# Kernel optimization log

Measured on AMD Instinct MI355X. Metric: run time of the kernel, lower is better.

The kernel has to match this reference:

```python
import jax, jax.numpy as jnp
import numpy as np

EMBED_DIM = 1024
HEADS = 16
HEAD_DIM = EMBED_DIM // HEADS


def setup_inputs() -> dict:
    key = jax.random.key(0)
    ks = jax.random.split(key, 9)
    D = EMBED_DIM
    s = 1.0 / np.sqrt(D)
    x = jax.random.normal(ks[0], (4, 2048, D), dtype=jnp.float32)
    Wq = jax.random.uniform(ks[1], (D, D), jnp.float32, -s, s)
    bq = jnp.zeros((D,), jnp.float32)
    Wk = jax.random.uniform(ks[2], (D, D), jnp.float32, -s, s)
    bk = jnp.zeros((D,), jnp.float32)
    Wv = jax.random.uniform(ks[3], (D, D), jnp.float32, -s, s)
    bv = jnp.zeros((D,), jnp.float32)
    Wo = jax.random.uniform(ks[4], (D, D), jnp.float32, -s, s)
    bo = jnp.zeros((D,), jnp.float32)
    gamma = jnp.ones((D,), jnp.float32)
    beta = jnp.zeros((D,), jnp.float32)
    return {"x": x, "Wq": Wq, "bq": bq, "Wk": Wk, "bk": bk,
            "Wv": Wv, "bv": bv, "Wo": Wo, "bo": bo,
            "gamma": gamma, "beta": beta}


def reference(x, Wq, bq, Wk, bk, Wv, bv, Wo, bo, gamma, beta):
    B, S, D = x.shape
    H, Dh = HEADS, HEAD_DIM
    # projections -> [B, H, S, Dh]
    q = (x @ Wq + bq).reshape(B, S, H, Dh).transpose(0, 2, 1, 3)
    k = (x @ Wk + bk).reshape(B, S, H, Dh).transpose(0, 2, 1, 3)
    v = (x @ Wv + bv).reshape(B, S, H, Dh).transpose(0, 2, 1, 3)
    scores = jnp.einsum('bhqd,bhkd->bhqk', q, k) / jnp.sqrt(jnp.float32(Dh))
    attn = jax.nn.softmax(scores, axis=-1)  # dropout is identity in eval
    ctx = jnp.einsum('bhqk,bhkd->bhqd', attn, v)
    ctx = ctx.transpose(0, 2, 1, 3).reshape(B, S, D)
    out = ctx @ Wo + bo
    # residual + LayerNorm (eps=1e-5, torch default)
    h = out + x
    mu = jnp.mean(h, axis=-1, keepdims=True)
    var = jnp.mean(jnp.square(h - mu), axis=-1, keepdims=True)
    return (h - mu) * jax.lax.rsqrt(var + 1e-5) * gamma + beta
```

## Files before the change

### kernel.cpp

```cpp
#include <hip/hip_runtime.h>
#include <hip/hip_bf16.h>
#include <stdint.h>

typedef short sh4 __attribute__((ext_vector_type(4)));
typedef short sh8 __attribute__((ext_vector_type(8)));
typedef float fl4 __attribute__((ext_vector_type(4)));
typedef float f32x4 __attribute__((ext_vector_type(4)));
typedef float f32x16 __attribute__((ext_vector_type(16)));
typedef uint32_t u32x4 __attribute__((ext_vector_type(4)));

static __device__ __forceinline__ short f2bf(float f) {
  union { float f; uint32_t u; } v;
  v.f = f;
  uint32_t r = v.u + 0x7fffu + ((v.u >> 16) & 1u);
  return (short)(r >> 16);
}

static __device__ __forceinline__ uint32_t cvt_pk_bf16(float a, float b) {
  uint32_t r;
  asm("v_cvt_pk_bf16_f32 %0, %1, %2" : "=v"(r) : "v"(a), "v"(b));
  return r;
}

static __device__ __forceinline__ void pl32swap(uint32_t& a, uint32_t& b) {
  asm volatile("v_permlane32_swap_b32 %0, %1" : "+v"(a), "+v"(b));
}

static __device__ __forceinline__ void gload_lds16(const void* g, void* l) {
  __builtin_amdgcn_global_load_lds((const __attribute__((address_space(1))) void*)g,
                                   (__attribute__((address_space(3))) void*)l, 16, 0, 0);
}

__global__ __launch_bounds__(256) void k_wt(const float* __restrict__ Wq, const float* __restrict__ Wk,
                                            const float* __restrict__ Wv, const float* __restrict__ Wo,
                                            short* __restrict__ Tq, short* __restrict__ Tk,
                                            short* __restrict__ Tv, short* __restrict__ To) {
  const float* W = blockIdx.z == 0 ? Wq : blockIdx.z == 1 ? Wk : blockIdx.z == 2 ? Wv : Wo;
  short* T = blockIdx.z == 0 ? Tq : blockIdx.z == 1 ? Tk : blockIdx.z == 2 ? Tv : To;
  __shared__ float tile[32][33];
  int n0 = blockIdx.x * 32, k0 = blockIdx.y * 32;
  int tx = threadIdx.x, ty = threadIdx.y;
#pragma unroll
  for (int p = 0; p < 4; p++) tile[ty + 8 * p][tx] = W[(size_t)(k0 + ty + 8 * p) * 1024 + n0 + tx];
  __syncthreads();
#pragma unroll
  for (int p = 0; p < 4; p++) T[(size_t)(n0 + ty + 8 * p) * 1024 + k0 + tx] = f2bf(tile[tx][ty + 8 * p]);
}

__global__ __launch_bounds__(256) void k_cvtx(const float* __restrict__ x, short* __restrict__ o) {
  int i = blockIdx.x * 256 + threadIdx.x;
  fl4 v = ((const fl4*)x)[i];
  sh4 r;
#pragma unroll
  for (int j = 0; j < 4; j++) r[j] = f2bf(v[j]);
  ((sh4*)o)[i] = r;
}

__global__ __launch_bounds__(256) void k_qkv3(const short* __restrict__ A, const short* __restrict__ WT3,
                                              const float* __restrict__ bq, const float* __restrict__ bk,
                                              const float* __restrict__ bv, short* __restrict__ Qo,
                                              short* __restrict__ Ko, short* __restrict__ Vo, float qscale) {
  __shared__ __align__(16) short As[128 * 32];
  __shared__ __align__(16) short Bs[128 * 32];
  const int m0 = blockIdx.y * 128, n0 = blockIdx.x * 128;
  const int sec = n0 >> 10;
  const float* bias = sec == 0 ? bq : sec == 1 ? bk : bv;
  short* Out = sec == 0 ? Qo : sec == 1 ? Ko : Vo;
  const float scale = sec == 0 ? qscale : 1.f;
  const int t = threadIdx.x;
  const int lane = t & 63, w = t >> 6;
  const int wr = w >> 1, wc = w & 1;
  const int l15 = lane & 15, g = lane >> 4;
  f32x4 acc[4][4];
#pragma unroll
  for (int mi = 0; mi < 4; mi++)
#pragma unroll
    for (int ni = 0; ni < 4; ni++) acc[mi][ni] = (f32x4){0.f, 0.f, 0.f, 0.f};
  for (int kk = 0; kk < 1024; kk += 32) {
    __syncthreads();
    {
      int r0 = w * 32;
#pragma unroll
      for (int i = 0; i < 2; i++) {
        int row = r0 + i * 16 + (lane >> 2);
        gload_lds16(&A[(size_t)(m0 + row) * 1024 + kk + (lane & 3) * 8], &As[(r0 + i * 16) * 32]);
        gload_lds16(&WT3[(size_t)(n0 + row) * 1024 + kk + (lane & 3) * 8], &Bs[(r0 + i * 16) * 32]);
      }
    }
    __syncthreads();
    sh8 a[4], b[4];
#pragma unroll
    for (int i = 0; i < 4; i++) a[i] = *(sh8*)&As[(wr * 64 + i * 16 + l15) * 32 + g * 8];
#pragma unroll
    for (int i = 0; i < 4; i++) b[i] = *(sh8*)&Bs[(wc * 64 + i * 16 + l15) * 32 + g * 8];
#pragma unroll
    for (int mi = 0; mi < 4; mi++)
#pragma unroll
      for (int ni = 0; ni < 4; ni++)
        acc[mi][ni] = __builtin_amdgcn_mfma_f32_16x16x32_bf16(a[mi], b[ni], acc[mi][ni], 0, 0, 0);
  }
#pragma unroll
  for (int ni = 0; ni < 4; ni++) {
    int col = n0 + wc * 64 + ni * 16 + l15;
    int nn = col & 1023;
    float bvv = bias[nn];
    int h = nn >> 6, dh = nn & 63;
#pragma unroll
    for (int mi = 0; mi < 4; mi++) {
#pragma unroll
      for (int r = 0; r < 4; r++) {
        int m = m0 + wr * 64 + mi * 16 + g * 4 + r;
        int bb = m >> 11, s = m & 2047;
        float val = (acc[mi][ni][r] + bvv) * scale;
        size_t off = (sec == 2) ? ((((size_t)bb * 16 + h) * 64 + dh) * 2048 + s)
                                : ((((size_t)bb * 16 + h) * 2048 + s) * 64 + dh);
        Out[off] = f2bf(val);
      }
    }
  }
}

__global__ __launch_bounds__(256) void k_oproj(const short* __restrict__ A, const short* __restrict__ BT,
                                               const float* __restrict__ bias, const float* __restrict__ X,
                                               float* __restrict__ Out) {
  __shared__ __align__(16) short As[128 * 32];
  __shared__ __align__(16) short Bs[128 * 32];
  const int m0 = blockIdx.y * 128, n0 = blockIdx.x * 128;
  const int t = threadIdx.x;
  const int lane = t & 63, w = t >> 6;
  const int wr = w >> 1, wc = w & 1;
  const int l15 = lane & 15, g = lane >> 4;
  f32x4 acc[4][4];
#pragma unroll
  for (int mi = 0; mi < 4; mi++)
#pragma unroll
    for (int ni = 0; ni < 4; ni++) acc[mi][ni] = (f32x4){0.f, 0.f, 0.f, 0.f};
  for (int kk = 0; kk < 1024; kk += 32) {
    __syncthreads();
    {
      int r0 = w * 32;
#pragma unroll
      for (int i = 0; i < 2; i++) {
        int row = r0 + i * 16 + (lane >> 2);
        gload_lds16(&A[(size_t)(m0 + row) * 1024 + kk + (lane & 3) * 8], &As[(r0 + i * 16) * 32]);
        gload_lds16(&BT[(size_t)(n0 + row) * 1024 + kk + (lane & 3) * 8], &Bs[(r0 + i * 16) * 32]);
      }
    }
    __syncthreads();
    sh8 a[4], b[4];
#pragma unroll
    for (int i = 0; i < 4; i++) a[i] = *(sh8*)&As[(wr * 64 + i * 16 + l15) * 32 + g * 8];
#pragma unroll
    for (int i = 0; i < 4; i++) b[i] = *(sh8*)&Bs[(wc * 64 + i * 16 + l15) * 32 + g * 8];
#pragma unroll
    for (int mi = 0; mi < 4; mi++)
#pragma unroll
      for (int ni = 0; ni < 4; ni++)
        acc[mi][ni] = __builtin_amdgcn_mfma_f32_16x16x32_bf16(a[mi], b[ni], acc[mi][ni], 0, 0, 0);
  }
#pragma unroll
  for (int ni = 0; ni < 4; ni++) {
    int col = n0 + wc * 64 + ni * 16 + l15;
    float bv = bias[col];
#pragma unroll
    for (int mi = 0; mi < 4; mi++) {
#pragma unroll
      for (int r = 0; r < 4; r++) {
        int m = m0 + wr * 64 + mi * 16 + g * 4 + r;
        Out[(size_t)m * 1024 + col] = acc[mi][ni][r] + bv + X[(size_t)m * 1024 + col];
      }
    }
  }
}

__global__ __launch_bounds__(256, 3) void k_attn(const short* __restrict__ Q, const short* __restrict__ K,
                                                 const short* __restrict__ Vt, short* __restrict__ CTX) {
  const int nid = (blockIdx.x & 7) * 128 + (blockIdx.x >> 3);
  const int qb = nid & 15, h = (nid >> 4) & 15, b = nid >> 8;
  const int q0 = qb * 128;
  const size_t ho = (((size_t)b * 16 + h) * 2048) * 64;
  const short* Qh = Q + ho;
  const short* Kh = K + ho;
  const short* Vh = Vt + ho;
  __shared__ __align__(16) short Ks[2][64 * 64];
  __shared__ __align__(16) short Vs[2][64 * 64];
  const int t = threadIdx.x, lane = t & 63, w = t >> 6;
  const int l31 = lane & 31, hi = lane >> 5;
  const int swz = (l31 & 7) << 4;

  sh8 qreg[4];
#pragma unroll
  for (int ks = 0; ks < 4; ks++)
    qreg[ks] = *(const sh8*)&Qh[(size_t)(q0 + w * 32 + l31) * 64 + ks * 16 + hi * 8];

  f32x16 oc0, oc1;
#pragma unroll
  for (int r = 0; r < 16; r++) { oc0[r] = 0.f; oc1[r] = 0.f; }
  float m_s = -1e30f, l_s = 0.f;

  auto stage = [&](int kt, int buf) {
    int r0 = w * 16;
#pragma unroll
    for (int i = 0; i < 2; i++) {
      int row = r0 + i * 8 + (lane >> 3);
      int colb = ((lane & 7) * 16) ^ ((row & 7) << 4);
      gload_lds16(&Kh[(size_t)(kt * 64 + row) * 64 + (colb >> 1)], &Ks[buf][(r0 + i * 8) * 64]);
      gload_lds16(&Vh[(size_t)row * 2048 + kt * 64 + (colb >> 1)], &Vs[buf][(r0 + i * 8) * 64]);
    }
  };

  stage(0, 0);
  __syncthreads();

  for (int kt = 0; kt < 32; kt++) {
    int buf = kt & 1;
    if (kt + 1 < 32) stage(kt + 1, buf ^ 1);

    f32x16 s0, s1;
#pragma unroll
    for (int r = 0; r < 16; r++) { s0[r] = 0.f; s1[r] = 0.f; }
    __builtin_amdgcn_s_setprio(1);
#pragma unroll
    for (int ks = 0; ks < 4; ks++) {
      sh8 ak0 = *(sh8*)((char*)&Ks[buf][0] + l31 * 128 + ((ks * 32 + hi * 16) ^ swz));
      sh8 ak1 = *(sh8*)((char*)&Ks[buf][0] + (32 + l31) * 128 + ((ks * 32 + hi * 16) ^ swz));
      s0 = __builtin_amdgcn_mfma_f32_32x32x16_bf16(ak0, qreg[ks], s0, 0, 0, 0);
      s1 = __builtin_amdgcn_mfma_f32_32x32x16_bf16(ak1, qreg[ks], s1, 0, 0, 0);
    }
    __builtin_amdgcn_s_setprio(0);

    float pm = s0[0];
#pragma unroll
    for (int r = 1; r < 16; r++) pm = fmaxf(pm, s0[r]);
#pragma unroll
    for (int r = 0; r < 16; r++) pm = fmaxf(pm, s1[r]);
    pm = fmaxf(pm, __shfl_xor(pm, 32));
    if (__any(pm > m_s + 8.f)) {
      float mn = fmaxf(m_s, pm);
      float rs = __builtin_amdgcn_exp2f(m_s - mn);
      m_s = mn;
      l_s *= rs;
#pragma unroll
      for (int r = 0; r < 16; r++) { oc0[r] *= rs; oc1[r] *= rs; }
    }
    float ps = 0.f;
#pragma unroll
    for (int r = 0; r < 16; r++) { s0[r] = __builtin_amdgcn_exp2f(s0[r] - m_s); ps += s0[r]; }
#pragma unroll
    for (int r = 0; r < 16; r++) { s1[r] = __builtin_amdgcn_exp2f(s1[r] - m_s); ps += s1[r]; }
    l_s += ps;

    u32x4 pw0, pw1, pw2, pw3;
    {
      uint32_t a0 = cvt_pk_bf16(s0[0], s0[1]), a1 = cvt_pk_bf16(s0[2], s0[3]);
      uint32_t b0 = cvt_pk_bf16(s0[4], s0[5]), b1 = cvt_pk_bf16(s0[6], s0[7]);
      uint32_t c0 = cvt_pk_bf16(s0[8], s0[9]), c1 = cvt_pk_bf16(s0[10], s0[11]);
      uint32_t d0 = cvt_pk_bf16(s0[12], s0[13]), d1 = cvt_pk_bf16(s0[14], s0[15]);
      pl32swap(a0, b0); pl32swap(a1, b1); pl32swap(c0, d0); pl32swap(c1, d1);
      pw0 = (u32x4){a0, a1, b0, b1};
      pw1 = (u32x4){c0, c1, d0, d1};
      a0 = cvt_pk_bf16(s1[0], s1[1]); a1 = cvt_pk_bf16(s1[2], s1[3]);
      b0 = cvt_pk_bf16(s1[4], s1[5]); b1 = cvt_pk_bf16(s1[6], s1[7]);
      c0 = cvt_pk_bf16(s1[8], s1[9]); c1 = cvt_pk_bf16(s1[10], s1[11]);
      d0 = cvt_pk_bf16(s1[12], s1[13]); d1 = cvt_pk_bf16(s1[14], s1[15]);
      pl32swap(a0, b0); pl32swap(a1, b1); pl32swap(c0, d0); pl32swap(c1, d1);
      pw2 = (u32x4){a0, a1, b0, b1};
      pw3 = (u32x4){c0, c1, d0, d1};
    }
    sh8 pb0 = __builtin_bit_cast(sh8, pw0), pb1 = __builtin_bit_cast(sh8, pw1);
    sh8 pb2 = __builtin_bit_cast(sh8, pw2), pb3 = __builtin_bit_cast(sh8, pw3);

    __builtin_amdgcn_s_setprio(1);
#pragma unroll
    for (int ks = 0; ks < 4; ks++) {
      sh8 pb = ks == 0 ? pb0 : ks == 1 ? pb1 : ks == 2 ? pb2 : pb3;
      sh8 av0 = *(sh8*)((char*)&Vs[buf][0] + l31 * 128 + ((ks * 32 + hi * 16) ^ swz));
      sh8 av1 = *(sh8*)((char*)&Vs[buf][0] + (32 + l31) * 128 + ((ks * 32 + hi * 16) ^ swz));
      oc0 = __builtin_amdgcn_mfma_f32_32x32x16_bf16(av0, pb, oc0, 0, 0, 0);
      oc1 = __builtin_amdgcn_mfma_f32_32x32x16_bf16(av1, pb, oc1, 0, 0, 0);
    }
    __builtin_amdgcn_s_setprio(0);
    __syncthreads();
  }

  l_s += __shfl_xor(l_s, 32);
  float li = 1.f / l_s;
  int s = q0 + w * 32 + l31;
  size_t obase = (((size_t)b * 2048 + s) * 16 + h) * 64;
#pragma unroll
  for (int rq = 0; rq < 4; rq++) {
    uint2 dd;
    dd.x = cvt_pk_bf16(oc0[4 * rq] * li, oc0[4 * rq + 1] * li);
    dd.y = cvt_pk_bf16(oc0[4 * rq + 2] * li, oc0[4 * rq + 3] * li);
    *(uint2*)&CTX[obase + rq * 8 + hi * 4] = dd;
    dd.x = cvt_pk_bf16(oc1[4 * rq] * li, oc1[4 * rq + 1] * li);
    dd.y = cvt_pk_bf16(oc1[4 * rq + 2] * li, oc1[4 * rq + 3] * li);
    *(uint2*)&CTX[obase + 32 + rq * 8 + hi * 4] = dd;
  }
}

__global__ __launch_bounds__(256) void k_ln(float* __restrict__ Out, const float* __restrict__ gamma,
                                            const float* __restrict__ beta) {
  int row = blockIdx.x * 4 + (threadIdx.x >> 6);
  int lane = threadIdx.x & 63;
  float* p = Out + (size_t)row * 1024;
  fl4 v[4];
  float s = 0.f, s2 = 0.f;
#pragma unroll
  for (int j = 0; j < 4; j++) {
    v[j] = *(fl4*)&p[lane * 4 + j * 256];
#pragma unroll
    for (int e = 0; e < 4; e++) { s += v[j][e]; s2 += v[j][e] * v[j][e]; }
  }
#pragma unroll
  for (int off = 1; off < 64; off <<= 1) {
    s += __shfl_xor(s, off);
    s2 += __shfl_xor(s2, off);
  }
  float mu = s * (1.f / 1024.f);
  float var = s2 * (1.f / 1024.f) - mu * mu;
  float inv = rsqrtf(var + 1e-5f);
#pragma unroll
  for (int j = 0; j < 4; j++) {
    fl4 r;
#pragma unroll
    for (int e = 0; e < 4; e++) {
      int c = lane * 4 + j * 256 + e;
      r[e] = (v[j][e] - mu) * inv * gamma[c] + beta[c];
    }
    *(fl4*)&p[lane * 4 + j * 256] = r;
  }
}

extern "C" void kernel_launch(void* const* d_in, const int* in_sizes, int n_in,
                              void* d_out, int out_size, void* d_ws, size_t ws_size,
                              hipStream_t stream) {
  (void)in_sizes; (void)n_in; (void)out_size; (void)ws_size;
  const float* x = (const float*)d_in[0];
  const float* Wq = (const float*)d_in[1];
  const float* bq = (const float*)d_in[2];
  const float* Wk = (const float*)d_in[3];
  const float* bk = (const float*)d_in[4];
  const float* Wv = (const float*)d_in[5];
  const float* bv = (const float*)d_in[6];
  const float* Wo = (const float*)d_in[7];
  const float* bo = (const float*)d_in[8];
  const float* gamma = (const float*)d_in[9];
  const float* beta = (const float*)d_in[10];
  float* out = (float*)d_out;
  char* ws = (char*)d_ws;
  short* xbf = (short*)(ws);
  short* wtq = (short*)(ws + (16ull << 20));
  short* wtk = (short*)(ws + (18ull << 20));
  short* wtv = (short*)(ws + (20ull << 20));
  short* wto = (short*)(ws + (22ull << 20));
  short* qb  = (short*)(ws + (24ull << 20));
  short* kbuf = (short*)(ws + (40ull << 20));
  short* vbuf = (short*)(ws + (56ull << 20));
  short* ctx = (short*)(ws + (72ull << 20));

  const float QSCALE = 0.125f * 1.44269504088896f;

  k_wt<<<dim3(32, 32, 4), dim3(32, 8), 0, stream>>>(Wq, Wk, Wv, Wo, wtq, wtk, wtv, wto);
  k_cvtx<<<8192, 256, 0, stream>>>(x, xbf);
  k_qkv3<<<dim3(24, 64), 256, 0, stream>>>(xbf, wtq, bq, bk, bv, qb, kbuf, vbuf, QSCALE);
  k_attn<<<1024, 256, 0, stream>>>(qb, kbuf, vbuf, ctx);
  k_oproj<<<dim3(8, 64), 256, 0, stream>>>(ctx, wto, bo, x, out);
  k_ln<<<2048, 256, 0, stream>>>(out, gamma, beta);
}
```

Measured before the change: 244.9 us.

## Double-buffer LDS in projection GEMMs and remap blocks for XCD locality

```diff
diff --git a/kernel.cpp b/kernel.cpp
--- a/kernel.cpp
+++ b/kernel.cpp
@@ -60,9 +60,10 @@
                                               const float* __restrict__ bq, const float* __restrict__ bk,
                                               const float* __restrict__ bv, short* __restrict__ Qo,
                                               short* __restrict__ Ko, short* __restrict__ Vo, float qscale) {
-  __shared__ __align__(16) short As[128 * 32];
-  __shared__ __align__(16) short Bs[128 * 32];
-  const int m0 = blockIdx.y * 128, n0 = blockIdx.x * 128;
+  __shared__ __align__(16) short As[2][128 * 32];
+  __shared__ __align__(16) short Bs[2][128 * 32];
+  const int xcd = blockIdx.x & 7, j = blockIdx.x >> 3;
+  const int m0 = (xcd + 8 * (j & 7)) * 128, n0 = (j >> 3) * 128;
   const int sec = n0 >> 10;
   const float* bias = sec == 0 ? bq : sec == 1 ? bk : bv;
   short* Out = sec == 0 ? Qo : sec == 1 ? Ko : Vo;
@@ -76,28 +77,35 @@
   for (int mi = 0; mi < 4; mi++)
 #pragma unroll
     for (int ni = 0; ni < 4; ni++) acc[mi][ni] = (f32x4){0.f, 0.f, 0.f, 0.f};
-  for (int kk = 0; kk < 1024; kk += 32) {
-    __syncthreads();
-    {
-      int r0 = w * 32;
-#pragma unroll
-      for (int i = 0; i < 2; i++) {
-        int row = r0 + i * 16 + (lane >> 2);
-        gload_lds16(&A[(size_t)(m0 + row) * 1024 + kk + (lane & 3) * 8], &As[(r0 + i * 16) * 32]);
-        gload_lds16(&WT3[(size_t)(n0 + row) * 1024 + kk + (lane & 3) * 8], &Bs[(r0 + i * 16) * 32]);
-      }
-    }
-    __syncthreads();
+
+  auto stage = [&](int kk, int buf) {
+    int r0 = w * 32;
+#pragma unroll
+    for (int i = 0; i < 2; i++) {
+      int row = r0 + i * 16 + (lane >> 2);
+      gload_lds16(&A[(size_t)(m0 + row) * 1024 + kk + (lane & 3) * 8], &As[buf][(r0 + i * 16) * 32]);
+      gload_lds16(&WT3[(size_t)(n0 + row) * 1024 + kk + (lane & 3) * 8], &Bs[buf][(r0 + i * 16) * 32]);
+    }
+  };
+
+  stage(0, 0);
+  __syncthreads();
+  for (int it = 0; it < 32; it++) {
+    int buf = it & 1;
+    if (it + 1 < 32) stage((it + 1) * 32, buf ^ 1);
     sh8 a[4], b[4];
 #pragma unroll
-    for (int i = 0; i < 4; i++) a[i] = *(sh8*)&As[(wr * 64 + i * 16 + l15) * 32 + g * 8];
-#pragma unroll
-    for (int i = 0; i < 4; i++) b[i] = *(sh8*)&Bs[(wc * 64 + i * 16 + l15) * 32 + g * 8];
+    for (int i = 0; i < 4; i++) a[i] = *(sh8*)&As[buf][(wr * 64 + i * 16 + l15) * 32 + g * 8];
+#pragma unroll
+    for (int i = 0; i < 4; i++) b[i] = *(sh8*)&Bs[buf][(wc * 64 + i * 16 + l15) * 32 + g * 8];
+    __builtin_amdgcn_s_setprio(1);
 #pragma unroll
     for (int mi = 0; mi < 4; mi++)
 #pragma unroll
       for (int ni = 0; ni < 4; ni++)
         acc[mi][ni] = __builtin_amdgcn_mfma_f32_16x16x32_bf16(a[mi], b[ni], acc[mi][ni], 0, 0, 0);
+    __builtin_amdgcn_s_setprio(0);
+    __syncthreads();
   }
 #pragma unroll
   for (int ni = 0; ni < 4; ni++) {
@@ -123,9 +131,10 @@
 __global__ __launch_bounds__(256) void k_oproj(const short* __restrict__ A, const short* __restrict__ BT,
                                                const float* __restrict__ bias, const float* __restrict__ X,
                                                float* __restrict__ Out) {
-  __shared__ __align__(16) short As[128 * 32];
-  __shared__ __align__(16) short Bs[128 * 32];
-  const int m0 = blockIdx.y * 128, n0 = blockIdx.x * 128;
+  __shared__ __align__(16) short As[2][128 * 32];
+  __shared__ __align__(16) short Bs[2][128 * 32];
+  const int xcd = blockIdx.x & 7, j = blockIdx.x >> 3;
+  const int m0 = (xcd + 8 * (j & 7)) * 128, n0 = (j >> 3) * 128;
   const int t = threadIdx.x;
   const int lane = t & 63, w = t >> 6;
   const int wr = w >> 1, wc = w & 1;
@@ -135,28 +144,35 @@
   for (int mi = 0; mi < 4; mi++)
 #pragma unroll
     for (int ni = 0; ni < 4; ni++) acc[mi][ni] = (f32x4){0.f, 0.f, 0.f, 0.f};
-  for (int kk = 0; kk < 1024; kk += 32) {
-    __syncthreads();
-    {
-      int r0 = w * 32;
-#pragma unroll
-      for (int i = 0; i < 2; i++) {
-        int row = r0 + i * 16 + (lane >> 2);
-        gload_lds16(&A[(size_t)(m0 + row) * 1024 + kk + (lane & 3) * 8], &As[(r0 + i * 16) * 32]);
-        gload_lds16(&BT[(size_t)(n0 + row) * 1024 + kk + (lane & 3) * 8], &Bs[(r0 + i * 16) * 32]);
-      }
-    }
-    __syncthreads();
+
+  auto stage = [&](int kk, int buf) {
+    int r0 = w * 32;
+#pragma unroll
+    for (int i = 0; i < 2; i++) {
+      int row = r0 + i * 16 + (lane >> 2);
+      gload_lds16(&A[(size_t)(m0 + row) * 1024 + kk + (lane & 3) * 8], &As[buf][(r0 + i * 16) * 32]);
+      gload_lds16(&BT[(size_t)(n0 + row) * 1024 + kk + (lane & 3) * 8], &Bs[buf][(r0 + i * 16) * 32]);
+    }
+  };
+
+  stage(0, 0);
+  __syncthreads();
+  for (int it = 0; it < 32; it++) {
+    int buf = it & 1;
+    if (it + 1 < 32) stage((it + 1) * 32, buf ^ 1);
     sh8 a[4], b[4];
 #pragma unroll
-    for (int i = 0; i < 4; i++) a[i] = *(sh8*)&As[(wr * 64 + i * 16 + l15) * 32 + g * 8];
-#pragma unroll
-    for (int i = 0; i < 4; i++) b[i] = *(sh8*)&Bs[(wc * 64 + i * 16 + l15) * 32 + g * 8];
+    for (int i = 0; i < 4; i++) a[i] = *(sh8*)&As[buf][(wr * 64 + i * 16 + l15) * 32 + g * 8];
+#pragma unroll
+    for (int i = 0; i < 4; i++) b[i] = *(sh8*)&Bs[buf][(wc * 64 + i * 16 + l15) * 32 + g * 8];
+    __builtin_amdgcn_s_setprio(1);
 #pragma unroll
     for (int mi = 0; mi < 4; mi++)
 #pragma unroll
       for (int ni = 0; ni < 4; ni++)
         acc[mi][ni] = __builtin_amdgcn_mfma_f32_16x16x32_bf16(a[mi], b[ni], acc[mi][ni], 0, 0, 0);
+    __builtin_amdgcn_s_setprio(0);
+    __syncthreads();
   }
 #pragma unroll
   for (int ni = 0; ni < 4; ni++) {
@@ -363,8 +379,8 @@
 
   k_wt<<<dim3(32, 32, 4), dim3(32, 8), 0, stream>>>(Wq, Wk, Wv, Wo, wtq, wtk, wtv, wto);
   k_cvtx<<<8192, 256, 0, stream>>>(x, xbf);
-  k_qkv3<<<dim3(24, 64), 256, 0, stream>>>(xbf, wtq, bq, bk, bv, qb, kbuf, vbuf, QSCALE);
+  k_qkv3<<<1536, 256, 0, stream>>>(xbf, wtq, bq, bk, bv, qb, kbuf, vbuf, QSCALE);
   k_attn<<<1024, 256, 0, stream>>>(qb, kbuf, vbuf, ctx);
-  k_oproj<<<dim3(8, 64), 256, 0, stream>>>(ctx, wto, bo, x, out);
+  k_oproj<<<512, 256, 0, stream>>>(ctx, wto, bo, x, out);
   k_ln<<<2048, 256, 0, stream>>>(out, gamma, beta);
 }
```

After: 237.9 us. 1.03x faster.
